# Optimization experiments

Measured on AMD Instinct MI355X. Metric: run time of the kernel, lower is better.

The kernel has to match this reference:

```python
import jax, jax.numpy as jnp
import numpy as np

T = 1.0  # temperature

def _free_energy(v, W, b, c):
    # v: [B, V]; W: [V, H]; b: [V]; c: [H]
    vW = v @ W                                  # [B, H]
    W_colsum = W.sum(axis=0)                    # [H]
    negF_normal = (v * b).sum(-1) - jax.nn.softplus(vW + c).sum(-1)
    negF_flip = ((1.0 - v) * b).sum(-1) - jax.nn.softplus(W_colsum - vW + c).sum(-1)
    negF = jnp.stack([negF_normal, negF_flip], axis=-1)  # [B, 2]
    return -T * jax.nn.logsumexp(negF / T, axis=-1)      # [B]

def _gibbs_chain(v0, W, b, c, key, k):
    B = v0.shape[0]
    key, k0 = jax.random.split(key)
    u0 = jax.random.bernoulli(k0, 0.5, (B, 1)).astype(v0.dtype)
    b_sum = b.sum()

    def step(carry, _):
        v, u, key = carry
        key, k1, k2, k3 = jax.random.split(key, 4)
        v_branch = u * v + (1.0 - u) * (1.0 - v)
        h = jax.random.bernoulli(k1, jax.nn.sigmoid(v_branch @ W + c)).astype(v.dtype)  # [B,H]
        a = h @ W.T                                                                     # [B,V]
        vb = (v * b).sum(-1)
        va = (v * a).sum(-1)
        dE = -b_sum - a.sum(-1) + 2.0 * vb + 2.0 * va
        u_new = jax.random.bernoulli(k2, jax.nn.sigmoid(dE)).astype(v.dtype)[:, None]
        v_new = jax.random.bernoulli(k3, jax.nn.sigmoid(a + b)).astype(v.dtype)
        v = u_new * v_new + (1.0 - u_new) * (1.0 - v_new)
        return (v, u_new, key), None

    (v_model, _, _), _ = jax.lax.scan(step, (v0, u0, key), None, length=k)
    return v_model

def setup_inputs() -> dict:
    key = jax.random.key(0)
    kv, kw = jax.random.split(key)
    B, V, H = 8192, 1024, 1024
    v_data = jnp.round(jax.random.uniform(kv, (B, V), dtype=jnp.float32))  # binary 0/1
    W = 0.01 * jax.random.normal(kw, (V, H), dtype=jnp.float32)
    b = jnp.zeros((V,), dtype=jnp.float32)
    c = jnp.zeros((H,), dtype=jnp.float32)
    return {"v_data": v_data, "W": W, "b": b, "c": c, "seed": 0}

def reference(v_data, W, b, c, seed):
    K = 10  # Gibbs steps
    key = jax.random.key(seed)
    v_model = _gibbs_chain(v_data, W, b, c, key, K)
    v_model = jax.lax.stop_gradient(v_model)  # .detach() in torch
    loss = _free_energy(v_data, W, b, c).mean() - _free_energy(v_model, W, b, c).mean()
    return loss
```

## Files before the change

### kernel.cpp

```cpp
#include <hip/hip_runtime.h>
#include <hip/hip_bf16.h>
#include <stdint.h>
#include <math.h>


static constexpr int Bn = 8192;
static constexpr int Vn = 1024;
static constexpr int Hn = 1024;
static constexpr int KSTEPS = 10;

typedef _Float16 f16;
typedef f16   f16x4 __attribute__((ext_vector_type(4)));
typedef f16   f16x8 __attribute__((ext_vector_type(8)));
typedef float f32x4 __attribute__((ext_vector_type(4)));

#define GLOBAL_LOAD_LDS16(g, l)                                              \
  __builtin_amdgcn_global_load_lds(                                          \
      (const __attribute__((address_space(1))) uint32_t*)(g),                \
      (__attribute__((address_space(3))) uint32_t*)(l), 16, 0, 0)

__device__ __forceinline__ uint32_t rotl32(uint32_t x, int d) {
  return (x << d) | (x >> (32 - d));
}

__device__ __forceinline__ void tf2x32(uint32_t k0, uint32_t k1,
                                       uint32_t x0, uint32_t x1,
                                       uint32_t& o0, uint32_t& o1) {
  uint32_t k2 = k0 ^ k1 ^ 0x1BD11BDAu;
#define TFR(r) { x0 += x1; x1 = rotl32(x1, (r)); x1 ^= x0; }
  x0 += k0; x1 += k1;
  TFR(13) TFR(15) TFR(26) TFR(6)
  x0 += k1; x1 += k2 + 1u;
  TFR(17) TFR(29) TFR(16) TFR(24)
  x0 += k2; x1 += k0 + 2u;
  TFR(13) TFR(15) TFR(26) TFR(6)
  x0 += k0; x1 += k1 + 3u;
  TFR(17) TFR(29) TFR(16) TFR(24)
  x0 += k1; x1 += k2 + 4u;
  TFR(13) TFR(15) TFR(26) TFR(6)
  x0 += k2; x1 += k0 + 5u;
#undef TFR
  o0 = x0; o1 = x1;
}

__device__ __forceinline__ float rng_u01(uint2 key, uint32_t idx) {
  uint32_t o0, o1;
  tf2x32(key.x, key.y, 0u, idx, o0, o1);
  uint32_t bits = o0 ^ o1;
  return __uint_as_float((bits >> 9) | 0x3F800000u) - 1.0f;
}

__device__ __forceinline__ float bern_fast(float z, float r01) {
  float e = __expf(-z);
  return (__builtin_fmaf(r01, e, r01) < 1.0f) ? 1.f : 0.f;
}
__device__ __forceinline__ float softplus_fast(float x) {
  return fmaxf(x, 0.f) + __logf(1.f + __expf(-fabsf(x)));
}

__global__ void prep_keys(const int* __restrict__ seedp, uint2* __restrict__ keys) {
  if (threadIdx.x != 0 || blockIdx.x != 0) return;
  uint32_t seed = (uint32_t)(*seedp);
  uint2 key = make_uint2(0u, seed);
  uint2 nk, kk;
  tf2x32(key.x, key.y, 0u, 0u, nk.x, nk.y);
  tf2x32(key.x, key.y, 0u, 1u, kk.x, kk.y);
  keys[0] = kk;
  key = nk;
  for (int s = 0; s < KSTEPS; ++s) {
    uint2 t0, t1, t2, t3;
    tf2x32(key.x, key.y, 0u, 0u, t0.x, t0.y);
    tf2x32(key.x, key.y, 0u, 1u, t1.x, t1.y);
    tf2x32(key.x, key.y, 0u, 2u, t2.x, t2.y);
    tf2x32(key.x, key.y, 0u, 3u, t3.x, t3.y);
    key = t0;
    keys[1 + 3*s] = t1;
    keys[2 + 3*s] = t2;
    keys[3 + 3*s] = t3;
  }
}

__global__ __launch_bounds__(256) void colsum_part(
    const float* __restrict__ W, float* __restrict__ part) {
  const int bx = blockIdx.x, t = threadIdx.x;
  float s0 = 0.f, s1 = 0.f, s2 = 0.f, s3 = 0.f;
#pragma unroll
  for (int r = 0; r < 16; ++r) {
    const float* row = W + (size_t)(bx * 16 + r) * Hn;
    s0 += row[t]; s1 += row[t + 256]; s2 += row[t + 512]; s3 += row[t + 768];
  }
  float* p = part + (size_t)bx * Hn;
  p[t] = s0; p[t + 256] = s1; p[t + 512] = s2; p[t + 768] = s3;
}

__global__ __launch_bounds__(256) void colsum_red(
    const float* __restrict__ part, float* __restrict__ cs) {
  const int col = blockIdx.x * 256 + threadIdx.x;
  float s = 0.f;
#pragma unroll
  for (int k = 0; k < 64; ++k) s += part[(size_t)k * Hn + col];
  cs[col] = s;
}

__global__ void bsum_k(const float* __restrict__ bvec, float* __restrict__ bs) {
  __shared__ float sb[4];
  float s = 0.f;
  for (int i = threadIdx.x; i < Vn; i += 256) s += bvec[i];
  for (int off = 32; off > 0; off >>= 1) s += __shfl_down(s, off, 64);
  int wv = threadIdx.x >> 6, ln = threadIdx.x & 63;
  if (ln == 0) sb[wv] = s;
  __syncthreads();
  if (threadIdx.x == 0) bs[0] = sb[0] + sb[1] + sb[2] + sb[3];
}

__global__ __launch_bounds__(256) void cast_W(
    const float* __restrict__ W, f16* __restrict__ Wf, f16* __restrict__ WTf) {
  __shared__ f16 tile[64][65];
  const int j0 = blockIdx.x * 64, i0 = blockIdx.y * 64;
  const int tx = threadIdx.x & 63, tg = threadIdx.x >> 6;
#pragma unroll 4
  for (int rr = 0; rr < 16; ++rr) {
    const int row = tg * 16 + rr;
    float w = W[(size_t)(i0 + row) * Hn + j0 + tx];
    f16 hw = (f16)w;
    Wf[(size_t)(i0 + row) * Hn + j0 + tx] = hw;
    tile[row][tx] = hw;
  }
  __syncthreads();
#pragma unroll 4
  for (int rr = 0; rr < 16; ++rr) {
    const int row = tg * 16 + rr;
    WTf[(size_t)(j0 + row) * Vn + i0 + tx] = tile[tx][row];
  }
}

__global__ void u0_init(const uint2* __restrict__ keys, float* __restrict__ u0) {
  int b = blockIdx.x * 256 + threadIdx.x;
  float r01 = rng_u01(keys[0], (uint32_t)b);
  u0[b] = (r01 < 0.5f) ? 1.f : 0.f;
}

__global__ __launch_bounds__(256) void cast_vx(
    const float* __restrict__ vd, const float* __restrict__ u0,
    const float* __restrict__ bvec, f16* __restrict__ x,
    float* __restrict__ pXB0) {
  const int row = blockIdx.x;
  const int t = threadIdx.x;
  const float uo = u0[row];
  const float4 d  = ((const float4*)(vd + (size_t)row * Vn))[t];
  const float4 bv = ((const float4*)bvec)[t];
  float xv[4] = { d.x, d.y, d.z, d.w };
  if (uo <= 0.5f) { xv[0]=1.f-xv[0]; xv[1]=1.f-xv[1]; xv[2]=1.f-xv[2]; xv[3]=1.f-xv[3]; }
  f16x4 o = { (f16)xv[0], (f16)xv[1], (f16)xv[2], (f16)xv[3] };
  *(f16x4*)(x + (size_t)row * Vn + t * 4) = o;
  float xb = xv[0]*bv.x + xv[1]*bv.y + xv[2]*bv.z + xv[3]*bv.w;
#pragma unroll
  for (int m = 1; m < 8; m <<= 1) xb += __shfl_xor(xb, m, 64);
  if ((t & 7) == 0) pXB0[(size_t)row * 32 + (t >> 3)] = xb;
}

template <int EPI>
__global__ __launch_bounds__(256, 8) void gemm_s(
    const f16* __restrict__ A, const f16* __restrict__ Bm,
    f16* __restrict__ outH, f16* __restrict__ xnew,
    const float* __restrict__ bvec, const float* __restrict__ cvec,
    const float* __restrict__ colsum,
    float* __restrict__ pA, float* __restrict__ pXA, float* __restrict__ pXBn,
    float* __restrict__ pSA, float* __restrict__ pSB,
    const uint2* __restrict__ keys, int keyIdx)
{
  constexpr int N = 1024, K = 1024, BK = 64;
  __shared__ alignas(16) f16 As[64 * BK];
  __shared__ alignas(16) f16 Bs[64 * BK];

  const int t = threadIdx.x, wave = t >> 6, lane = t & 63;
  const int l15 = lane & 15, quad = lane >> 4;
  const int m0 = blockIdx.x * 64, n0 = blockIdx.y * 64;
  const int wm = (wave >> 1) * 32, wn = (wave & 1) * 32;

  const int rbase = lane >> 3;
  const int gch   = (lane & 7) ^ rbase;
  const f16* gA = A  + (size_t)(m0 + wave * 16 + rbase) * K + gch * 8;
  const f16* gB = Bm + (size_t)(n0 + wave * 16 + rbase) * K + gch * 8;
  f16* lA = As + wave * 16 * BK;
  f16* lB = Bs + wave * 16 * BK;

  const int swz = l15 & 7;
  const int oA  = (wm + l15) * BK;
  const int oB  = (wn + l15) * BK;

  f32x4 acc[2][2] = {};

  for (int k0 = 0; k0 < K; k0 += BK) {
    GLOBAL_LOAD_LDS16(gA + k0,         lA);
    GLOBAL_LOAD_LDS16(gA + k0 + 8 * K, lA + 8 * BK);
    GLOBAL_LOAD_LDS16(gB + k0,         lB);
    GLOBAL_LOAD_LDS16(gB + k0 + 8 * K, lB + 8 * BK);
    __syncthreads();

#pragma unroll
    for (int kc = 0; kc < 2; ++kc) {
      const int fc = ((kc * 4 + quad) ^ swz) * 8;
      f16x8 af[2], bf[2];
#pragma unroll
      for (int i = 0; i < 2; ++i) {
        af[i] = *(const f16x8*)(&As[oA + i * 16 * BK + fc]);
        bf[i] = *(const f16x8*)(&Bs[oB + i * 16 * BK + fc]);
      }
#pragma unroll
      for (int mt = 0; mt < 2; ++mt)
#pragma unroll
        for (int nt = 0; nt < 2; ++nt)
          acc[mt][nt] = __builtin_amdgcn_mfma_f32_16x16x32_f16(af[mt], bf[nt], acc[mt][nt], 0, 0, 0);
    }
    __syncthreads();
  }

  const int slot = blockIdx.y * 2 + (wave & 1);

  if constexpr (EPI == 1 || EPI == 2) {
    const uint2 key = keys[keyIdx];
    float csv[2], cvv[2];
#pragma unroll
    for (int nt = 0; nt < 2; ++nt) {
      const int gn = n0 + wn + nt * 16 + l15;
      csv[nt] = colsum[gn];
      cvv[nt] = cvec[gn];
    }
#pragma unroll
    for (int mt = 0; mt < 2; ++mt)
#pragma unroll
      for (int r = 0; r < 4; ++r) {
        const int gm = m0 + wm + mt * 16 + quad * 4 + r;
        float pa = 0.f, pxa = 0.f, sa = 0.f, sb = 0.f;
#pragma unroll
        for (int nt = 0; nt < 2; ++nt) {
          const int gn = n0 + wn + nt * 16 + l15;
          const float val = acc[mt][nt][r];
          float r01 = rng_u01(key, (uint32_t)(gm * N + gn));
          float hq  = bern_fast(val + cvv[nt], r01);
          outH[(size_t)gm * N + gn] = (f16)hq;
          pa  += hq * csv[nt];
          pxa += hq * val;
          if constexpr (EPI == 2) {
            sa += softplus_fast(val + cvv[nt]);
            sb += softplus_fast(csv[nt] - val + cvv[nt]);
          }
        }
#pragma unroll
        for (int m = 1; m < 16; m <<= 1) {
          pa  += __shfl_xor(pa,  m, 64);
          pxa += __shfl_xor(pxa, m, 64);
          if constexpr (EPI == 2) {
            sa += __shfl_xor(sa, m, 64);
            sb += __shfl_xor(sb, m, 64);
          }
        }
        if (l15 == 0) {
          pA [(size_t)gm * 32 + slot] = pa;
          pXA[(size_t)gm * 32 + slot] = pxa;
          if constexpr (EPI == 2) {
            pSA[(size_t)gm * 32 + slot] = sa;
            pSB[(size_t)gm * 32 + slot] = sb;
          }
        }
      }
  } else if constexpr (EPI == 3) {
    const uint2 key = keys[keyIdx];
    float bb[2];
#pragma unroll
    for (int nt = 0; nt < 2; ++nt) bb[nt] = bvec[n0 + wn + nt * 16 + l15];
#pragma unroll
    for (int mt = 0; mt < 2; ++mt)
#pragma unroll
      for (int r = 0; r < 4; ++r) {
        const int gm = m0 + wm + mt * 16 + quad * 4 + r;
        float pxb = 0.f;
#pragma unroll
        for (int nt = 0; nt < 2; ++nt) {
          const int gn = n0 + wn + nt * 16 + l15;
          const float aval = acc[mt][nt][r];
          float r01 = rng_u01(key, (uint32_t)(gm * N + gn));
          float xq  = bern_fast(aval + bb[nt], r01);
          xnew[(size_t)gm * N + gn] = (f16)xq;
          pxb += xq * bb[nt];
        }
#pragma unroll
        for (int m = 1; m < 16; m <<= 1) pxb += __shfl_xor(pxb, m, 64);
        if (l15 == 0) pXBn[(size_t)gm * 32 + slot] = pxb;
      }
  } else {
    float csv[2], cvv[2];
#pragma unroll
    for (int nt = 0; nt < 2; ++nt) {
      const int gn = n0 + wn + nt * 16 + l15;
      csv[nt] = colsum[gn];
      cvv[nt] = cvec[gn];
    }
#pragma unroll
    for (int mt = 0; mt < 2; ++mt)
#pragma unroll
      for (int r = 0; r < 4; ++r) {
        const int gm = m0 + wm + mt * 16 + quad * 4 + r;
        float sa = 0.f, sb = 0.f;
#pragma unroll
        for (int nt = 0; nt < 2; ++nt) {
          const float val = acc[mt][nt][r];
          sa += softplus_fast(val + cvv[nt]);
          sb += softplus_fast(csv[nt] - val + cvv[nt]);
        }
#pragma unroll
        for (int m = 1; m < 16; m <<= 1) {
          sa += __shfl_xor(sa, m, 64);
          sb += __shfl_xor(sb, m, 64);
        }
        if (l15 == 0) {
          pSA[(size_t)gm * 32 + slot] = sa;
          pSB[(size_t)gm * 32 + slot] = sb;
        }
      }
  }
}

__global__ __launch_bounds__(256) void u_chain(
    const float* __restrict__ pA, const float* __restrict__ pXA,
    const float* __restrict__ pXB, const float* __restrict__ bsum,
    const uint2* __restrict__ keys, const float* __restrict__ u0,
    float* __restrict__ uF)
{
  const int t = threadIdx.x, wave = t >> 6, lane = t & 63;
  const int r2 = lane >> 5, slot = lane & 31;
  const int row = blockIdx.x * 8 + wave * 2 + r2;
  const float bs = bsum[0];
  float uo = u0[row];
  for (int s = 0; s < KSTEPS; ++s) {
    const size_t o = (size_t)s * 32 * Bn + (size_t)row * 32 + slot;
    float sa  = pA [o];
    float sxa = pXA[o];
    float sxb = pXB[o];
#pragma unroll
    for (int m = 1; m < 32; m <<= 1) {
      sa  += __shfl_xor(sa,  m, 64);
      sxa += __shfl_xor(sxa, m, 64);
      sxb += __shfl_xor(sxb, m, 64);
    }
    const float va = (uo > 0.5f) ? sxa : sa - sxa;
    const float vb = (uo > 0.5f) ? sxb : bs - sxb;
    const float dE = -bs - sa + 2.f * vb + 2.f * va;
    uo = bern_fast(dE, rng_u01(keys[2 + 3 * s], (uint32_t)row));
  }
  if (slot == 0) uF[row] = uo;
}

__device__ __forceinline__ float fe_eval(float SA, float SB, float xb,
                                         float uo, float bs) {
  float S1 = (uo > 0.5f) ? SA : SB;
  float S2 = (uo > 0.5f) ? SB : SA;
  float vb = (uo > 0.5f) ? xb : bs - xb;
  float negn = vb - S1;
  float negf = (bs - vb) - S2;
  float mx = fmaxf(negn, negf);
  return -(mx + logf(expf(negn - mx) + expf(negf - mx)));
}

__global__ __launch_bounds__(256) void fe_finish(
    const float* __restrict__ SA0, const float* __restrict__ SB0,
    const float* __restrict__ xb0,
    const float* __restrict__ SAF, const float* __restrict__ SBF,
    const float* __restrict__ xbF,
    const float* __restrict__ u0, const float* __restrict__ uF,
    const float* __restrict__ bsum,
    float* __restrict__ Fd, float* __restrict__ Fm)
{
  const int t = threadIdx.x, wave = t >> 6, lane = t & 63;
  const int r2 = lane >> 5, slot = lane & 31;
  const int row = blockIdx.x * 8 + wave * 2 + r2;
  const size_t o = (size_t)row * 32 + slot;
  const float bs = bsum[0];
  float a0 = SA0[o], b0 = SB0[o], x0 = xb0[o];
  float aF = SAF[o], bF = SBF[o], xF = xbF[o];
#pragma unroll
  for (int m = 1; m < 32; m <<= 1) {
    a0 += __shfl_xor(a0, m, 64);  b0 += __shfl_xor(b0, m, 64);
    x0 += __shfl_xor(x0, m, 64);  aF += __shfl_xor(aF, m, 64);
    bF += __shfl_xor(bF, m, 64);  xF += __shfl_xor(xF, m, 64);
  }
  if (slot == 0) {
    Fd[row] = fe_eval(a0, b0, x0, u0[row], bs);
    Fm[row] = fe_eval(aF, bF, xF, uF[row], bs);
  }
}

__global__ __launch_bounds__(256) void finalize_k(
    const float* __restrict__ Fd, const float* __restrict__ Fm, float* __restrict__ out)
{
  __shared__ double sb[8];
  double sd = 0.0, sm = 0.0;
  for (int i = threadIdx.x; i < Bn; i += 256) { sd += (double)Fd[i]; sm += (double)Fm[i]; }
  for (int off = 32; off > 0; off >>= 1) { sd += __shfl_down(sd, off, 64); sm += __shfl_down(sm, off, 64); }
  const int wv = threadIdx.x >> 6, ln = threadIdx.x & 63;
  if (ln == 0) { sb[wv] = sd; sb[4 + wv] = sm; }
  __syncthreads();
  if (threadIdx.x == 0) {
    sd = sb[0] + sb[1] + sb[2] + sb[3];
    sm = sb[4] + sb[5] + sb[6] + sb[7];
    out[0] = (float)((sd - sm) / (double)Bn);
  }
}

extern "C" void kernel_launch(void* const* d_in, const int* in_sizes, int n_in,
                              void* d_out, int out_size, void* d_ws, size_t ws_size,
                              hipStream_t stream) {
  const float* v_data = (const float*)d_in[0];
  const float* W      = (const float*)d_in[1];
  const float* bvec   = (const float*)d_in[2];
  const float* cvec   = (const float*)d_in[3];
  const int*   seedp  = (const int*)d_in[4];
  float* out = (float*)d_out;

  char* ws = (char*)d_ws;
  size_t off = 0;
  auto alloc = [&](size_t bytes) -> void* {
    void* p = ws + off;
    off += (bytes + 255) & ~(size_t)255;
    return p;
  };
  f16*   xb0  = (f16*)alloc((size_t)Bn * Vn * 2);
  f16*   xb1  = (f16*)alloc((size_t)Bn * Vn * 2);
  f16*   h    = (f16*)alloc((size_t)Bn * Hn * 2);
  f16*   Wf   = (f16*)alloc((size_t)Vn * Hn * 2);
  f16*   WTf  = (f16*)alloc((size_t)Vn * Hn * 2);
  float* cpart  = (float*)alloc(64 * Hn * 4);
  float* colsum = (float*)alloc(Hn * 4);
  float* bsum   = (float*)alloc(256);
  uint2* keys   = (uint2*)alloc(64 * sizeof(uint2));
  float* u0     = (float*)alloc(Bn * 4);
  float* uF     = (float*)alloc(Bn * 4);
  float* pA     = (float*)alloc((size_t)KSTEPS * 32 * Bn * 4);
  float* pXA    = (float*)alloc((size_t)KSTEPS * 32 * Bn * 4);
  float* pXB    = (float*)alloc((size_t)(KSTEPS + 1) * 32 * Bn * 4);
  float* SA0    = (float*)alloc((size_t)32 * Bn * 4);
  float* SB0    = (float*)alloc((size_t)32 * Bn * 4);
  float* SAF    = (float*)alloc((size_t)32 * Bn * 4);
  float* SBF    = (float*)alloc((size_t)32 * Bn * 4);
  float* Fd     = (float*)alloc(Bn * 4);
  float* Fm     = (float*)alloc(Bn * 4);
  (void)ws_size; (void)in_sizes; (void)n_in; (void)out_size;

  prep_keys<<<1, 64, 0, stream>>>(seedp, keys);
  colsum_part<<<64, 256, 0, stream>>>(W, cpart);
  colsum_red<<<4, 256, 0, stream>>>(cpart, colsum);
  bsum_k<<<1, 256, 0, stream>>>(bvec, bsum);
  cast_W<<<dim3(Hn / 64, Vn / 64), 256, 0, stream>>>(W, Wf, WTf);
  u0_init<<<Bn / 256, 256, 0, stream>>>(keys, u0);
  cast_vx<<<Bn, 256, 0, stream>>>(v_data, u0, bvec, xb0, pXB);

  dim3 gg(Bn / 64, Hn / 64);
  f16* xs[2] = { xb0, xb1 };
  const size_t SL = (size_t)32 * Bn;

  for (int s = 0; s < KSTEPS; ++s) {
    if (s == 0) {
      gemm_s<2><<<gg, 256, 0, stream>>>(xs[0], WTf, h, nullptr, nullptr, cvec,
                                        colsum, pA, pXA, nullptr, SA0, SB0,
                                        keys, 1);
    } else {
      gemm_s<1><<<gg, 256, 0, stream>>>(xs[s & 1], WTf, h, nullptr, nullptr, cvec,
                                        colsum, pA + (size_t)s * SL,
                                        pXA + (size_t)s * SL, nullptr,
                                        nullptr, nullptr, keys, 1 + 3 * s);
    }
    gemm_s<3><<<gg, 256, 0, stream>>>(h, Wf, nullptr, xs[(s + 1) & 1], bvec,
                                      nullptr, nullptr, nullptr, nullptr,
                                      pXB + (size_t)(s + 1) * SL,
                                      nullptr, nullptr, keys, 3 + 3 * s);
  }

  gemm_s<4><<<gg, 256, 0, stream>>>(xs[KSTEPS & 1], WTf, nullptr, nullptr,
                                    nullptr, cvec, colsum, nullptr, nullptr,
                                    nullptr, SAF, SBF, keys, 0);

  u_chain<<<Bn / 8, 256, 0, stream>>>(pA, pXA, pXB, bsum, keys, u0, uF);
  fe_finish<<<Bn / 8, 256, 0, stream>>>(SA0, SB0, pXB,
                                        SAF, SBF, pXB + (size_t)KSTEPS * SL,
                                        u0, uF, bsum, Fd, Fm);
  finalize_k<<<1, 256, 0, stream>>>(Fd, Fm, out);
}
```

Measured before the change: 940.5 us.

## Enlarge GEMM M-tile and interleave Threefry RNG with the K loop

The GEMM tile grows from 64x64 to 128x64, so each wave holds 4x2 MFMA accumulators and the grid halves along M. The Threefry random numbers for the epilogue are now computed inside the fully unrolled K loop, two per iteration through a noinline helper, so their integer work can overlap the global-to-LDS loads and MFMAs instead of running serially after them. The 16-lane shuffle reductions become DPP adds, rotl uses alignbit, and the final barrier is dropped. The trade-off is much higher register pressure (32 stored randoms plus 32 accumulator floats per thread) and lower occupancy, with launch bounds cut from 8 to 4 blocks.

Result: faster. 856.3 us (-9.0%).

```diff
diff --git a/kernel.cpp b/kernel.cpp
--- a/kernel.cpp
+++ b/kernel.cpp
@@ -20,7 +20,7 @@
       (__attribute__((address_space(3))) uint32_t*)(l), 16, 0, 0)
 
 __device__ __forceinline__ uint32_t rotl32(uint32_t x, int d) {
-  return (x << d) | (x >> (32 - d));
+  return __builtin_amdgcn_alignbit(x, x, 32 - d);
 }
 
 __device__ __forceinline__ void tf2x32(uint32_t k0, uint32_t k1,
@@ -50,12 +50,33 @@
   return __uint_as_float((bits >> 9) | 0x3F800000u) - 1.0f;
 }
 
+__device__ __attribute__((noinline)) float2 rng2_u01(uint2 key, uint32_t i0,
+                                                     uint32_t i1) {
+  float2 r;
+  r.x = rng_u01(key, i0);
+  r.y = rng_u01(key, i1);
+  return r;
+}
+
 __device__ __forceinline__ float bern_fast(float z, float r01) {
   float e = __expf(-z);
   return (__builtin_fmaf(r01, e, r01) < 1.0f) ? 1.f : 0.f;
 }
 __device__ __forceinline__ float softplus_fast(float x) {
   return fmaxf(x, 0.f) + __logf(1.f + __expf(-fabsf(x)));
+}
+
+template <int CTRL>
+__device__ __forceinline__ float dpp_add16(float v) {
+  int x = __builtin_amdgcn_update_dpp(0, __float_as_int(v), CTRL, 0xF, 0xF, true);
+  return v + __int_as_float(x);
+}
+__device__ __forceinline__ float red16(float v) {
+  v = dpp_add16<0xB1>(v);
+  v = dpp_add16<0x4E>(v);
+  v = dpp_add16<0x141>(v);
+  v = dpp_add16<0x140>(v);
+  return v;
 }
 
 __global__ void prep_keys(const int* __restrict__ seedp, uint2* __restrict__ keys) {
@@ -160,7 +181,7 @@
 }
 
 template <int EPI>
-__global__ __launch_bounds__(256, 8) void gemm_s(
+__global__ __launch_bounds__(256, 4) void gemm_s(
     const f16* __restrict__ A, const f16* __restrict__ Bm,
     f16* __restrict__ outH, f16* __restrict__ xnew,
     const float* __restrict__ bvec, const float* __restrict__ cvec,
@@ -170,56 +191,77 @@
     const uint2* __restrict__ keys, int keyIdx)
 {
   constexpr int N = 1024, K = 1024, BK = 64;
-  __shared__ alignas(16) f16 As[64 * BK];
+  __shared__ alignas(16) f16 As[128 * BK];
   __shared__ alignas(16) f16 Bs[64 * BK];
 
   const int t = threadIdx.x, wave = t >> 6, lane = t & 63;
   const int l15 = lane & 15, quad = lane >> 4;
-  const int m0 = blockIdx.x * 64, n0 = blockIdx.y * 64;
-  const int wm = (wave >> 1) * 32, wn = (wave & 1) * 32;
+  const int m0 = blockIdx.x * 128, n0 = blockIdx.y * 64;
+  const int wm = (wave >> 1) * 64, wn = (wave & 1) * 32;
 
   const int rbase = lane >> 3;
   const int gch   = (lane & 7) ^ rbase;
-  const f16* gA = A  + (size_t)(m0 + wave * 16 + rbase) * K + gch * 8;
+  const f16* gA = A  + (size_t)(m0 + wave * 32 + rbase) * K + gch * 8;
   const f16* gB = Bm + (size_t)(n0 + wave * 16 + rbase) * K + gch * 8;
-  f16* lA = As + wave * 16 * BK;
+  f16* lA = As + wave * 32 * BK;
   f16* lB = Bs + wave * 16 * BK;
 
   const int swz = l15 & 7;
   const int oA  = (wm + l15) * BK;
   const int oB  = (wn + l15) * BK;
 
-  f32x4 acc[2][2] = {};
-
-  for (int k0 = 0; k0 < K; k0 += BK) {
-    GLOBAL_LOAD_LDS16(gA + k0,         lA);
-    GLOBAL_LOAD_LDS16(gA + k0 + 8 * K, lA + 8 * BK);
-    GLOBAL_LOAD_LDS16(gB + k0,         lB);
-    GLOBAL_LOAD_LDS16(gB + k0 + 8 * K, lB + 8 * BK);
+  uint2 key = make_uint2(0u, 0u);
+  if constexpr (EPI != 4) key = keys[keyIdx];
+
+  f32x4 acc[4][2] = {};
+  float r01v[32];
+
+#pragma unroll
+  for (int ki = 0; ki < 16; ++ki) {
+    const int k0 = ki * 64;
+#pragma unroll
+    for (int i = 0; i < 4; ++i)
+      GLOBAL_LOAD_LDS16(gA + k0 + i * 8 * K, lA + i * 8 * BK);
+#pragma unroll
+    for (int i = 0; i < 2; ++i)
+      GLOBAL_LOAD_LDS16(gB + k0 + i * 8 * K, lB + i * 8 * BK);
+    if constexpr (EPI != 4) {
+      uint32_t idx[2];
+#pragma unroll
+      for (int j = 0; j < 2; ++j) {
+        const int e  = ki * 2 + j;
+        const int mt = e >> 3, r = (e >> 1) & 3, nt = e & 1;
+        const int gm = m0 + wm + mt * 16 + quad * 4 + r;
+        const int gn = n0 + wn + nt * 16 + l15;
+        idx[j] = (uint32_t)(gm * N + gn);
+      }
+      float2 rv = rng2_u01(key, idx[0], idx[1]);
+      r01v[ki * 2 + 0] = rv.x;
+      r01v[ki * 2 + 1] = rv.y;
+    }
     __syncthreads();
-
 #pragma unroll
     for (int kc = 0; kc < 2; ++kc) {
       const int fc = ((kc * 4 + quad) ^ swz) * 8;
-      f16x8 af[2], bf[2];
-#pragma unroll
-      for (int i = 0; i < 2; ++i) {
+      f16x8 af[4], bf[2];
+#pragma unroll
+      for (int i = 0; i < 4; ++i)
         af[i] = *(const f16x8*)(&As[oA + i * 16 * BK + fc]);
+#pragma unroll
+      for (int i = 0; i < 2; ++i)
         bf[i] = *(const f16x8*)(&Bs[oB + i * 16 * BK + fc]);
-      }
-#pragma unroll
-      for (int mt = 0; mt < 2; ++mt)
+#pragma unroll
+      for (int mt = 0; mt < 4; ++mt)
 #pragma unroll
         for (int nt = 0; nt < 2; ++nt)
           acc[mt][nt] = __builtin_amdgcn_mfma_f32_16x16x32_f16(af[mt], bf[nt], acc[mt][nt], 0, 0, 0);
     }
-    __syncthreads();
+    if (ki < 15) __syncthreads();
   }
 
   const int slot = blockIdx.y * 2 + (wave & 1);
 
   if constexpr (EPI == 1 || EPI == 2) {
-    const uint2 key = keys[keyIdx];
     float csv[2], cvv[2];
 #pragma unroll
     for (int nt = 0; nt < 2; ++nt) {
@@ -228,7 +270,7 @@
       cvv[nt] = cvec[gn];
     }
 #pragma unroll
-    for (int mt = 0; mt < 2; ++mt)
+    for (int mt = 0; mt < 4; ++mt)
 #pragma unroll
       for (int r = 0; r < 4; ++r) {
         const int gm = m0 + wm + mt * 16 + quad * 4 + r;
@@ -237,7 +279,7 @@
         for (int nt = 0; nt < 2; ++nt) {
           const int gn = n0 + wn + nt * 16 + l15;
           const float val = acc[mt][nt][r];
-          float r01 = rng_u01(key, (uint32_t)(gm * N + gn));
+          const float r01 = r01v[mt * 8 + r * 2 + nt];
           float hq  = bern_fast(val + cvv[nt], r01);
           outH[(size_t)gm * N + gn] = (f16)hq;
           pa  += hq * csv[nt];
@@ -247,14 +289,11 @@
             sb += softplus_fast(csv[nt] - val + cvv[nt]);
           }
         }
-#pragma unroll
-        for (int m = 1; m < 16; m <<= 1) {
-          pa  += __shfl_xor(pa,  m, 64);
-          pxa += __shfl_xor(pxa, m, 64);
-          if constexpr (EPI == 2) {
-            sa += __shfl_xor(sa, m, 64);
-            sb += __shfl_xor(sb, m, 64);
-          }
+        pa  = red16(pa);
+        pxa = red16(pxa);
+        if constexpr (EPI == 2) {
+          sa = red16(sa);
+          sb = red16(sb);
         }
         if (l15 == 0) {
           pA [(size_t)gm * 32 + slot] = pa;
@@ -266,12 +305,11 @@
         }
       }
   } else if constexpr (EPI == 3) {
-    const uint2 key = keys[keyIdx];
     float bb[2];
 #pragma unroll
     for (int nt = 0; nt < 2; ++nt) bb[nt] = bvec[n0 + wn + nt * 16 + l15];
 #pragma unroll
-    for (int mt = 0; mt < 2; ++mt)
+    for (int mt = 0; mt < 4; ++mt)
 #pragma unroll
       for (int r = 0; r < 4; ++r) {
         const int gm = m0 + wm + mt * 16 + quad * 4 + r;
@@ -280,13 +318,12 @@
         for (int nt = 0; nt < 2; ++nt) {
           const int gn = n0 + wn + nt * 16 + l15;
           const float aval = acc[mt][nt][r];
-          float r01 = rng_u01(key, (uint32_t)(gm * N + gn));
+          const float r01 = r01v[mt * 8 + r * 2 + nt];
           float xq  = bern_fast(aval + bb[nt], r01);
           xnew[(size_t)gm * N + gn] = (f16)xq;
           pxb += xq * bb[nt];
         }
-#pragma unroll
-        for (int m = 1; m < 16; m <<= 1) pxb += __shfl_xor(pxb, m, 64);
+        pxb = red16(pxb);
         if (l15 == 0) pXBn[(size_t)gm * 32 + slot] = pxb;
       }
   } else {
@@ -298,7 +335,7 @@
       cvv[nt] = cvec[gn];
     }
 #pragma unroll
-    for (int mt = 0; mt < 2; ++mt)
+    for (int mt = 0; mt < 4; ++mt)
 #pragma unroll
       for (int r = 0; r < 4; ++r) {
         const int gm = m0 + wm + mt * 16 + quad * 4 + r;
@@ -309,11 +346,8 @@
           sa += softplus_fast(val + cvv[nt]);
           sb += softplus_fast(csv[nt] - val + cvv[nt]);
         }
-#pragma unroll
-        for (int m = 1; m < 16; m <<= 1) {
-          sa += __shfl_xor(sa, m, 64);
-          sb += __shfl_xor(sb, m, 64);
-        }
+        sa = red16(sa);
+        sb = red16(sb);
         if (l15 == 0) {
           pSA[(size_t)gm * 32 + slot] = sa;
           pSB[(size_t)gm * 32 + slot] = sb;
@@ -455,7 +489,7 @@
   u0_init<<<Bn / 256, 256, 0, stream>>>(keys, u0);
   cast_vx<<<Bn, 256, 0, stream>>>(v_data, u0, bvec, xb0, pXB);
 
-  dim3 gg(Bn / 64, Hn / 64);
+  dim3 gg(Bn / 128, Hn / 64);
   f16* xs[2] = { xb0, xb1 };
   const size_t SL = (size_t)32 * Bn;
 
```
